# Performance work log

Hardware: AMD Instinct MI355X
Metric: run time of the kernel (lower is better)

## Reference

```python
import jax, jax.numpy as jnp
import numpy as np

H = 256
B = 4096          # number of graphs / motifs in batch
NF = 131072       # focal atoms
NR = 262144       # residues
V = 8001          # vocab.size() + 1
TOPK = 5
DIST_THRESH = 6.0


def setup_inputs() -> dict:
    key = jax.random.key(0)
    ks = jax.random.split(key, 12)
    h_ctx_focal = jax.random.normal(ks[0], (NF, H), dtype=jnp.float32)
    pos_ctx_focal = jax.random.normal(ks[1], (NF, 3), dtype=jnp.float32)
    current_wid = jax.random.randint(ks[2], (B,), 0, V)
    current_atoms_batch = jnp.sort(jax.random.randint(ks[3], (NF,), 0, B))
    h_residue = jax.random.normal(ks[4], (NR, H), dtype=jnp.float32)
    residue_pos = jax.random.normal(ks[5], (NR, 3, 3), dtype=jnp.float32)
    amino_acid_batch = jnp.sort(jax.random.randint(ks[6], (NR,), 0, B))
    emb_weight = jax.random.normal(ks[7], (V, H), dtype=jnp.float32) * 0.02
    mlp_w1 = jax.random.normal(ks[8], (3 * H, H), dtype=jnp.float32) * (1.0 / np.sqrt(3 * H))
    mlp_b1 = jnp.zeros((H,), dtype=jnp.float32)
    mlp_w2 = jax.random.normal(ks[9], (H, H), dtype=jnp.float32) * (1.0 / np.sqrt(H))
    mlp_b2 = jnp.zeros((H,), dtype=jnp.float32)
    return {
        'h_ctx_focal': h_ctx_focal, 'pos_ctx_focal': pos_ctx_focal,
        'current_wid': current_wid, 'current_atoms_batch': current_atoms_batch,
        'h_residue': h_residue, 'residue_pos': residue_pos,
        'amino_acid_batch': amino_acid_batch, 'emb_weight': emb_weight,
        'mlp_w1': mlp_w1, 'mlp_b1': mlp_b1, 'mlp_w2': mlp_w2, 'mlp_b2': mlp_b2,
    }


def reference(h_ctx_focal, pos_ctx_focal, current_wid, current_atoms_batch,
              h_residue, residue_pos, amino_acid_batch,
              emb_weight, mlp_w1, mlp_b1, mlp_w2, mlp_b2):
    nB = current_wid.shape[0]
    # scatter_add over focal atoms -> [B, H]
    node_hiddens = jax.ops.segment_sum(h_ctx_focal, current_atoms_batch, num_segments=nB)
    # embedding lookup -> [B, H]
    motif_hiddens = emb_weight[current_wid]
    # scatter_mean of positions -> [B, 3]
    pos_sum = jax.ops.segment_sum(pos_ctx_focal, current_atoms_batch, num_segments=nB)
    counts = jax.ops.segment_sum(jnp.ones((pos_ctx_focal.shape[0],), jnp.float32),
                                 current_atoms_batch, num_segments=nB)
    center_pos = pos_sum / jnp.maximum(counts, 1.0)[:, None]
    # CA position of each residue, distance mask (< 6 A from motif center)
    ca_pos = residue_pos[:, 1, :]                                  # [NR, 3]
    dist = jnp.linalg.norm(ca_pos - center_pos[amino_acid_batch], axis=1)
    mask = dist < DIST_THRESH                                      # [NR]
    # masked scatter_add of residue embeddings -> [B, H]
    residue_emb = jax.ops.segment_sum(jnp.where(mask[:, None], h_residue, 0.0),
                                      amino_acid_batch, num_segments=nB)
    # motif MLP (2 layers) + projection onto embedding table
    pred_vecs = jnp.concatenate([node_hiddens, motif_hiddens, residue_emb], axis=-1)  # [B, 3H]
    h = jax.nn.relu(pred_vecs @ mlp_w1 + mlp_b1)
    mh = h @ mlp_w2 + mlp_b2                                        # [B, H]
    pred_scores = mh @ emb_weight.T                                 # [B, V]
    # top-k + random selection among top-k
    _, select_pool = jax.lax.top_k(pred_scores, TOPK)               # [B, k]
    idx = jax.random.randint(jax.random.key(1), (nB,), 0, TOPK)
    preds = jnp.take_along_axis(select_pool, idx[:, None], axis=1)[:, 0]
    return (pred_scores, preds)
```

## Files before the change

kernel.cpp:

```cpp
#include <hip/hip_runtime.h>
#include <hip/hip_bf16.h>
#include <cstdint>

#define HD   256
#define BSZ  4096
#define NFV  131072
#define NRV  262144
#define VV   8001
#define TOPKN 5
#define RBOFF (BSZ + 1)
#define EPAD 8064

typedef __attribute__((ext_vector_type(8))) short short8v;
typedef __attribute__((ext_vector_type(4))) float float4v;

__host__ __device__ __forceinline__ unsigned rotl32(unsigned v, int d) {
  return (v << d) | (v >> (32 - d));
}

__host__ __device__ __forceinline__ void threefry2x32(
    unsigned k0, unsigned k1, unsigned x0, unsigned x1,
    unsigned& o0, unsigned& o1) {
  unsigned ks2 = k0 ^ k1 ^ 0x1BD11BDAu;
  x0 += k0; x1 += k1;
  x0 += x1; x1 = rotl32(x1, 13); x1 ^= x0;
  x0 += x1; x1 = rotl32(x1, 15); x1 ^= x0;
  x0 += x1; x1 = rotl32(x1, 26); x1 ^= x0;
  x0 += x1; x1 = rotl32(x1,  6); x1 ^= x0;
  x0 += k1; x1 += ks2 + 1u;
  x0 += x1; x1 = rotl32(x1, 17); x1 ^= x0;
  x0 += x1; x1 = rotl32(x1, 29); x1 ^= x0;
  x0 += x1; x1 = rotl32(x1, 16); x1 ^= x0;
  x0 += x1; x1 = rotl32(x1, 24); x1 ^= x0;
  x0 += ks2; x1 += k0 + 2u;
  x0 += x1; x1 = rotl32(x1, 13); x1 ^= x0;
  x0 += x1; x1 = rotl32(x1, 15); x1 ^= x0;
  x0 += x1; x1 = rotl32(x1, 26); x1 ^= x0;
  x0 += x1; x1 = rotl32(x1,  6); x1 ^= x0;
  x0 += k0; x1 += k1 + 3u;
  x0 += x1; x1 = rotl32(x1, 17); x1 ^= x0;
  x0 += x1; x1 = rotl32(x1, 29); x1 ^= x0;
  x0 += x1; x1 = rotl32(x1, 16); x1 ^= x0;
  x0 += x1; x1 = rotl32(x1, 24); x1 ^= x0;
  x0 += k1; x1 += ks2 + 4u;
  x0 += x1; x1 = rotl32(x1, 13); x1 ^= x0;
  x0 += x1; x1 = rotl32(x1, 15); x1 ^= x0;
  x0 += x1; x1 = rotl32(x1, 26); x1 ^= x0;
  x0 += x1; x1 = rotl32(x1,  6); x1 ^= x0;
  x0 += ks2; x1 += k0 + 5u;
  o0 = x0; o1 = x1;
}

__device__ __forceinline__ unsigned short f2bf(float f) {
  unsigned u = __float_as_uint(f);
  unsigned r = (u + 0x7FFFu + ((u >> 16) & 1u)) >> 16;
  return (unsigned short)r;
}
__device__ __forceinline__ float bf2f(unsigned short s) {
  return __uint_as_float(((unsigned)s) << 16);
}

__device__ __forceinline__ int lower_bound_i(const int* __restrict__ a, int n, int v) {
  int lo = 0, hi = n;
  while (lo < hi) { int m = (lo + hi) >> 1; if (a[m] < v) lo = m + 1; else hi = m; }
  return lo;
}

__global__ __launch_bounds__(256) void seg_bounds_kernel(
    const int* __restrict__ ab, const int* __restrict__ rb,
    int* __restrict__ bounds) {
  int i = blockIdx.x * 256 + threadIdx.x;
  if (i <= BSZ) bounds[i] = lower_bound_i(ab, NFV, i);
  else if (i <= 2 * BSZ + 1) bounds[i] = lower_bound_i(rb, NRV, i - RBOFF);
}

__global__ __launch_bounds__(256) void convert_emb_kernel(
    const float* __restrict__ emb, unsigned short* __restrict__ ehi,
    unsigned short* __restrict__ elo) {
  size_t i = ((size_t)blockIdx.x * 256 + threadIdx.x) * 4;
  int row = (int)(i >> 8);
  float f[4] = {0.f, 0.f, 0.f, 0.f};
  if (row < VV) {
    float4 v = *reinterpret_cast<const float4*>(&emb[i]);
    f[0] = v.x; f[1] = v.y; f[2] = v.z; f[3] = v.w;
  }
  unsigned short h[4], l[4];
#pragma unroll
  for (int j = 0; j < 4; ++j) {
    h[j] = f2bf(f[j]);
    l[j] = f2bf(f[j] - bf2f(h[j]));
  }
  *reinterpret_cast<uint2*>(&ehi[i]) = *reinterpret_cast<uint2*>(h);
  *reinterpret_cast<uint2*>(&elo[i]) = *reinterpret_cast<uint2*>(l);
}

__global__ __launch_bounds__(256) void mask_kernel(
    const float* __restrict__ pcf, const float* __restrict__ rpos,
    const int* __restrict__ bounds, unsigned char* __restrict__ mask) {
  int lane = threadIdx.x & 63;
  int b = blockIdx.x * 4 + (threadIdx.x >> 6);
  int a0 = bounds[b], a1 = bounds[b + 1];
  int r0 = bounds[RBOFF + b], r1 = bounds[RBOFF + b + 1];

  float cp = 0.f;
  if (lane < 3 && a0 < a1) {
    float nv = pcf[(size_t)a0 * 3 + lane];
    for (int aa = a0; aa < a1; ++aa) {
      float cv = nv;
      if (aa + 1 < a1) nv = pcf[(size_t)(aa + 1) * 3 + lane];
      cp += cv;
    }
  }
  if (lane < 3) cp = cp / fmaxf((float)(a1 - a0), 1.0f);
  float cx = __shfl(cp, 0), cy = __shfl(cp, 1), cz = __shfl(cp, 2);

  for (int r = r0 + lane; r < r1; r += 64) {
    float dx = rpos[(size_t)r * 9 + 3] - cx;
    float dy = rpos[(size_t)r * 9 + 4] - cy;
    float dz = rpos[(size_t)r * 9 + 5] - cz;
    mask[r] = (dx * dx + dy * dy + dz * dz < 36.0f) ? 1 : 0;
  }
}

__global__ __launch_bounds__(256) void fuse_seg_kernel(
    const float* __restrict__ hcf, const int* __restrict__ wid,
    const float* __restrict__ hres, const unsigned char* __restrict__ mask,
    const float* __restrict__ emb, const int* __restrict__ bounds,
    float* __restrict__ pred_vecs) {
  int lane = threadIdx.x & 63;
  int b = blockIdx.x * 4 + (threadIdx.x >> 6);
  int a0 = bounds[b], a1 = bounds[b + 1];
  int r0 = bounds[RBOFF + b], r1 = bounds[RBOFF + b + 1];
  size_t off = (size_t)lane * 4;

  float4v acc = 0.f;
  int a = a0;
  for (; a + 8 <= a1; a += 8) {
    float4v v[8];
#pragma unroll
    for (int j = 0; j < 8; ++j)
      v[j] = *reinterpret_cast<const float4v*>(&hcf[(size_t)(a + j) * HD + off]);
    acc += ((v[0] + v[1]) + (v[2] + v[3])) + ((v[4] + v[5]) + (v[6] + v[7]));
  }
  for (; a < a1; ++a)
    acc += *reinterpret_cast<const float4v*>(&hcf[(size_t)a * HD + off]);

  size_t o = (size_t)b * (3 * HD);
  *reinterpret_cast<float4v*>(&pred_vecs[o + off]) = acc;
  float4v mv = *reinterpret_cast<const float4v*>(&emb[(size_t)wid[b] * HD + off]);
  *reinterpret_cast<float4v*>(&pred_vecs[o + HD + off]) = mv;

  float4v racc = 0.f;
  int r = r0;
  for (; r < r1 && (r & 7); ++r) {
    float4v v = *reinterpret_cast<const float4v*>(&hres[(size_t)r * HD + off]);
    if (mask[r]) racc += v;
  }
  for (; r + 8 <= r1; r += 8) {
    uint2 mw = *reinterpret_cast<const uint2*>(&mask[r]);
    float4v v[8];
#pragma unroll
    for (int j = 0; j < 8; ++j)
      v[j] = *reinterpret_cast<const float4v*>(&hres[(size_t)(r + j) * HD + off]);
    float4v s0 = 0.f, s1 = 0.f, s2 = 0.f, s3 = 0.f;
    if (mw.x & 0x000000FFu) s0 += v[0];
    if (mw.x & 0x0000FF00u) s1 += v[1];
    if (mw.x & 0x00FF0000u) s2 += v[2];
    if (mw.x & 0xFF000000u) s3 += v[3];
    if (mw.y & 0x000000FFu) s0 += v[4];
    if (mw.y & 0x0000FF00u) s1 += v[5];
    if (mw.y & 0x00FF0000u) s2 += v[6];
    if (mw.y & 0xFF000000u) s3 += v[7];
    racc += (s0 + s1) + (s2 + s3);
  }
  for (; r < r1; ++r) {
    float4v v = *reinterpret_cast<const float4v*>(&hres[(size_t)r * HD + off]);
    if (mask[r]) racc += v;
  }
  *reinterpret_cast<float4v*>(&pred_vecs[o + 2 * HD + off]) = racc;
}

template <bool RELU, bool SPLIT>
__global__ __launch_bounds__(256) void gemm_kernel(
    const float* __restrict__ A, const float* __restrict__ B,
    const float* __restrict__ bias, float* __restrict__ C,
    unsigned short* __restrict__ Chi, unsigned short* __restrict__ Clo,
    int M, int N, int K) {
  __shared__ float As[16][64];
  __shared__ float Bs[16][64];
  int t = threadIdx.x;
  int bm = blockIdx.y * 64, bn = blockIdx.x * 64;
  int tx = t & 15, ty = t >> 4;
  float acc[4][4] = {};

  for (int k0 = 0; k0 < K; k0 += 16) {
    {
      int ar = t >> 2, ak = (t & 3) << 2;
      float4 av = *reinterpret_cast<const float4*>(&A[(size_t)(bm + ar) * K + k0 + ak]);
      As[ak + 0][ar] = av.x; As[ak + 1][ar] = av.y;
      As[ak + 2][ar] = av.z; As[ak + 3][ar] = av.w;
    }
    {
      int bk = t >> 4, bnn = (t & 15) << 2;
      float4 bv = *reinterpret_cast<const float4*>(&B[(size_t)(k0 + bk) * N + bn + bnn]);
      *reinterpret_cast<float4*>(&Bs[bk][bnn]) = bv;
    }
    __syncthreads();
#pragma unroll
    for (int kk = 0; kk < 16; ++kk) {
      float4 a = *reinterpret_cast<const float4*>(&As[kk][ty << 2]);
      float4 b = *reinterpret_cast<const float4*>(&Bs[kk][tx << 2]);
      float av4[4] = {a.x, a.y, a.z, a.w};
      float bv4[4] = {b.x, b.y, b.z, b.w};
#pragma unroll
      for (int i = 0; i < 4; ++i)
#pragma unroll
        for (int j = 0; j < 4; ++j)
          acc[i][j] = fmaf(av4[i], bv4[j], acc[i][j]);
    }
    __syncthreads();
  }

#pragma unroll
  for (int i = 0; i < 4; ++i) {
    int row = bm + (ty << 2) + i;
    if (SPLIT) {
      unsigned short h[4], l[4];
#pragma unroll
      for (int j = 0; j < 4; ++j) {
        float v = acc[i][j] + bias[bn + (tx << 2) + j];
        h[j] = f2bf(v);
        l[j] = f2bf(v - bf2f(h[j]));
      }
      size_t base = (size_t)row * N + bn + (tx << 2);
      *reinterpret_cast<uint2*>(&Chi[base]) = *reinterpret_cast<uint2*>(h);
      *reinterpret_cast<uint2*>(&Clo[base]) = *reinterpret_cast<uint2*>(l);
    } else {
#pragma unroll
      for (int j = 0; j < 4; ++j) {
        int col = bn + (tx << 2) + j;
        float v = acc[i][j] + bias[col];
        if (RELU) v = fmaxf(v, 0.f);
        C[(size_t)row * N + col] = v;
      }
    }
  }
}

#define SW(row, col) ((col) ^ (((row) & 7) << 3))

__global__ __launch_bounds__(256, 2) void score_gemm_kernel(
    const unsigned short* __restrict__ Ahg, const unsigned short* __restrict__ Alg,
    const unsigned short* __restrict__ Bhg, const unsigned short* __restrict__ Blg,
    float* __restrict__ C) {
  __shared__ __attribute__((aligned(16))) unsigned short Ah[128 * 64];
  __shared__ __attribute__((aligned(16))) unsigned short Al[128 * 64];
  __shared__ __attribute__((aligned(16))) unsigned short Bh[128 * 64];
  __shared__ __attribute__((aligned(16))) unsigned short Bl[128 * 64];

  int t = threadIdx.x;
  int bm = blockIdx.x * 128;
  int bn = blockIdx.y * 128;
  int lane = t & 63, wv = t >> 6;
  int wm = wv >> 1, wn = wv & 1;
  int lr = lane & 15, lg = lane >> 4;

  float4v acc[4][4] = {};

  int srow = t >> 1, scol = (t & 1) * 32;

  for (int kb = 0; kb < 256; kb += 64) {
#pragma unroll
    for (int j = 0; j < 4; ++j) {
      int c = scol + j * 8;
      int li = srow * 64 + SW(srow, c);
      size_t ga = (size_t)(bm + srow) * 256 + kb + c;
      size_t gb = (size_t)(bn + srow) * 256 + kb + c;
      *reinterpret_cast<short8v*>(&Ah[li]) = *reinterpret_cast<const short8v*>(&Ahg[ga]);
      *reinterpret_cast<short8v*>(&Al[li]) = *reinterpret_cast<const short8v*>(&Alg[ga]);
      *reinterpret_cast<short8v*>(&Bh[li]) = *reinterpret_cast<const short8v*>(&Bhg[gb]);
      *reinterpret_cast<short8v*>(&Bl[li]) = *reinterpret_cast<const short8v*>(&Blg[gb]);
    }
    __syncthreads();

#pragma unroll
    for (int ks = 0; ks < 2; ++ks) {
      int ko = ks * 32 + lg * 8;
      short8v aH[4], aL[4], bH[4], bL[4];
#pragma unroll
      for (int f = 0; f < 4; ++f) {
        int ra = wm * 64 + f * 16 + lr;
        int rb2 = wn * 64 + f * 16 + lr;
        aH[f] = *reinterpret_cast<const short8v*>(&Ah[ra * 64 + SW(ra, ko)]);
        aL[f] = *reinterpret_cast<const short8v*>(&Al[ra * 64 + SW(ra, ko)]);
        bH[f] = *reinterpret_cast<const short8v*>(&Bh[rb2 * 64 + SW(rb2, ko)]);
        bL[f] = *reinterpret_cast<const short8v*>(&Bl[rb2 * 64 + SW(rb2, ko)]);
      }
#pragma unroll
      for (int mf = 0; mf < 4; ++mf)
#pragma unroll
        for (int nf = 0; nf < 4; ++nf) {
          acc[mf][nf] = __builtin_amdgcn_mfma_f32_16x16x32_bf16(
              aH[mf], bH[nf], acc[mf][nf], 0, 0, 0);
          acc[mf][nf] = __builtin_amdgcn_mfma_f32_16x16x32_bf16(
              aH[mf], bL[nf], acc[mf][nf], 0, 0, 0);
          acc[mf][nf] = __builtin_amdgcn_mfma_f32_16x16x32_bf16(
              aL[mf], bH[nf], acc[mf][nf], 0, 0, 0);
        }
    }
    __syncthreads();
  }

#pragma unroll
  for (int mf = 0; mf < 4; ++mf)
#pragma unroll
    for (int nf = 0; nf < 4; ++nf) {
      int col = bn + wn * 64 + nf * 16 + lr;
      if (col < VV) {
#pragma unroll
        for (int rr = 0; rr < 4; ++rr) {
          int row = bm + wm * 64 + mf * 16 + lg * 4 + rr;
          C[(size_t)row * VV + col] = acc[mf][nf][rr];
        }
      }
    }
}

#define BETTER(av, ai, bv, bi) ((av) > (bv) || ((av) == (bv) && (ai) < (bi)))

__global__ __launch_bounds__(256) void topk_kernel(
    const float* __restrict__ scores, float* __restrict__ preds,
    unsigned k1a, unsigned k1b, unsigned k2a, unsigned k2b) {
  int lane = threadIdx.x & 63;
  int row = (blockIdx.x << 2) + (threadIdx.x >> 6);
  const float* s = scores + (size_t)row * VV;

  const float NEG = -__builtin_huge_valf();
  float v0 = NEG, v1 = NEG, v2 = NEG, v3 = NEG, v4 = NEG;
  int i0 = 0x7FFFFFFF, i1 = 0x7FFFFFFF, i2 = 0x7FFFFFFF, i3 = 0x7FFFFFFF, i4 = 0x7FFFFFFF;

  for (int v = lane; v < VV; v += 64) {
    float val = s[v];
    if (BETTER(val, v, v4, i4)) {
      if (BETTER(val, v, v3, i3)) {
        v4 = v3; i4 = i3;
        if (BETTER(val, v, v2, i2)) {
          v3 = v2; i3 = i2;
          if (BETTER(val, v, v1, i1)) {
            v2 = v1; i2 = i1;
            if (BETTER(val, v, v0, i0)) {
              v1 = v0; i1 = i0; v0 = val; i0 = v;
            } else { v1 = val; i1 = v; }
          } else { v2 = val; i2 = v; }
        } else { v3 = val; i3 = v; }
      } else { v4 = val; i4 = v; }
    }
  }

  int sel0, sel1, sel2, sel3, sel4;
#pragma unroll
  for (int p = 0; p < TOPKN; ++p) {
    float bv = v0; int bi = i0;
#pragma unroll
    for (int off = 32; off > 0; off >>= 1) {
      float ov = __shfl_xor(bv, off);
      int   oi = __shfl_xor(bi, off);
      if (BETTER(ov, oi, bv, bi)) { bv = ov; bi = oi; }
    }
    if (p == 0) sel0 = bi; else if (p == 1) sel1 = bi; else if (p == 2) sel2 = bi;
    else if (p == 3) sel3 = bi; else sel4 = bi;
    if (bi == i0) {
      v0 = v1; i0 = i1; v1 = v2; i1 = i2; v2 = v3; i2 = i3; v3 = v4; i3 = i4;
      v4 = NEG; i4 = 0x7FFFFFFF;
    }
  }

  if (lane == 0) {
    unsigned i = (unsigned)row;
    unsigned h0, h1, l0, l1;
    threefry2x32(k1a, k1b, 0u, i, h0, h1);
    threefry2x32(k2a, k2b, 0u, i, l0, l1);
    unsigned hb = h0 ^ h1;
    unsigned lb = l0 ^ l1;
    unsigned idx = ((hb % 5u) + (lb % 5u)) % 5u;
    int pick = (idx == 0) ? sel0 : (idx == 1) ? sel1 : (idx == 2) ? sel2
             : (idx == 3) ? sel3 : sel4;
    preds[row] = (float)pick;
  }
}

extern "C" void kernel_launch(void* const* d_in, const int* in_sizes, int n_in,
                              void* d_out, int out_size, void* d_ws, size_t ws_size,
                              hipStream_t stream) {
  const float* hcf  = (const float*)d_in[0];
  const float* pcf  = (const float*)d_in[1];
  const int*   wid  = (const int*)d_in[2];
  const int*   ab   = (const int*)d_in[3];
  const float* hres = (const float*)d_in[4];
  const float* rpos = (const float*)d_in[5];
  const int*   rb   = (const int*)d_in[6];
  const float* emb  = (const float*)d_in[7];
  const float* w1   = (const float*)d_in[8];
  const float* bb1  = (const float*)d_in[9];
  const float* w2   = (const float*)d_in[10];
  const float* bb2  = (const float*)d_in[11];

  float* out    = (float*)d_out;
  float* scores = out;
  float* preds  = out + (size_t)BSZ * VV;

  float* pred_vecs = out;
  float* hbuf      = out + (size_t)BSZ * 768;

  char* ws = (char*)d_ws;
  int*            bounds = (int*)(ws);
  unsigned char*  mask   = (unsigned char*)(ws + 0x10000);
  unsigned short* mh_hi  = (unsigned short*)(ws + 0x100000);
  unsigned short* mh_lo  = (unsigned short*)(ws + 0x300000);
  unsigned short* emb_hi = (unsigned short*)(ws + 0x500000);
  unsigned short* emb_lo = (unsigned short*)(ws + 0x900000);

  seg_bounds_kernel<<<(2 * (BSZ + 1) + 255) / 256, 256, 0, stream>>>(ab, rb, bounds);

  convert_emb_kernel<<<(EPAD * 256 / 4) / 256, 256, 0, stream>>>(emb, emb_hi, emb_lo);

  mask_kernel<<<BSZ / 4, 256, 0, stream>>>(pcf, rpos, bounds, mask);

  fuse_seg_kernel<<<BSZ / 4, 256, 0, stream>>>(
      hcf, wid, hres, mask, emb, bounds, pred_vecs);

  gemm_kernel<true, false><<<dim3(256 / 64, BSZ / 64), 256, 0, stream>>>(
      pred_vecs, w1, bb1, hbuf, nullptr, nullptr, BSZ, 256, 768);
  gemm_kernel<false, true><<<dim3(256 / 64, BSZ / 64), 256, 0, stream>>>(
      hbuf, w2, bb2, nullptr, mh_hi, mh_lo, BSZ, 256, 256);

  score_gemm_kernel<<<dim3(BSZ / 128, (VV + 127) / 128), 256, 0, stream>>>(
      mh_hi, mh_lo, emb_hi, emb_lo, scores);

  unsigned k1a, k1b, k2a, k2b;
  threefry2x32(0u, 1u, 0u, 0u, k1a, k1b);
  threefry2x32(0u, 1u, 0u, 1u, k2a, k2b);
  topk_kernel<<<BSZ / 4, 256, 0, stream>>>(scores, preds, k1a, k1b, k2a, k2b);
}
```

Measured before the change: 344.6 us.

## Move MLP GEMMs to split-bf16 MFMA and use direct global-to-LDS loads

Replaces the two fp32 SIMT MLP GEMMs with MFMA kernels that take operands split into bf16 hi/lo parts. The segment-sum kernel now writes pred_vecs already split, and the weights are transposed and split inside a new combined prep kernel that also absorbs the bounds and embedding conversion launches. The score GEMM switches to global_load_lds for direct-to-LDS staging and drops the XOR swizzle, which may bring back LDS bank conflicts. The three-product split-bf16 scheme slightly changes the arithmetic compared with fp32 FMA.

```diff
diff --git a/kernel.cpp b/kernel.cpp
--- a/kernel.cpp
+++ b/kernel.cpp
@@ -66,32 +66,54 @@
   return lo;
 }
 
-__global__ __launch_bounds__(256) void seg_bounds_kernel(
-    const int* __restrict__ ab, const int* __restrict__ rb,
-    int* __restrict__ bounds) {
-  int i = blockIdx.x * 256 + threadIdx.x;
-  if (i <= BSZ) bounds[i] = lower_bound_i(ab, NFV, i);
-  else if (i <= 2 * BSZ + 1) bounds[i] = lower_bound_i(rb, NRV, i - RBOFF);
-}
-
-__global__ __launch_bounds__(256) void convert_emb_kernel(
+__device__ __forceinline__ void gl16(const unsigned short* g, unsigned short* l) {
+  __builtin_amdgcn_global_load_lds(
+      (const __attribute__((address_space(1))) unsigned int*)g,
+      (__attribute__((address_space(3))) unsigned int*)l, 16, 0, 0);
+}
+
+__global__ __launch_bounds__(256) void prep_kernel(
+    const int* __restrict__ ab, const int* __restrict__ rb, int* __restrict__ bounds,
     const float* __restrict__ emb, unsigned short* __restrict__ ehi,
-    unsigned short* __restrict__ elo) {
-  size_t i = ((size_t)blockIdx.x * 256 + threadIdx.x) * 4;
-  int row = (int)(i >> 8);
-  float f[4] = {0.f, 0.f, 0.f, 0.f};
-  if (row < VV) {
-    float4 v = *reinterpret_cast<const float4*>(&emb[i]);
-    f[0] = v.x; f[1] = v.y; f[2] = v.z; f[3] = v.w;
-  }
-  unsigned short h[4], l[4];
-#pragma unroll
-  for (int j = 0; j < 4; ++j) {
-    h[j] = f2bf(f[j]);
-    l[j] = f2bf(f[j] - bf2f(h[j]));
-  }
-  *reinterpret_cast<uint2*>(&ehi[i]) = *reinterpret_cast<uint2*>(h);
-  *reinterpret_cast<uint2*>(&elo[i]) = *reinterpret_cast<uint2*>(l);
+    unsigned short* __restrict__ elo,
+    const float* __restrict__ w1, unsigned short* __restrict__ w1th,
+    unsigned short* __restrict__ w1tl,
+    const float* __restrict__ w2, unsigned short* __restrict__ w2th,
+    unsigned short* __restrict__ w2tl) {
+  int blk = blockIdx.x, t = threadIdx.x;
+  if (blk < 33) {
+    int i = blk * 256 + t;
+    if (i <= BSZ) bounds[i] = lower_bound_i(ab, NFV, i);
+    else if (i <= 2 * BSZ + 1) bounds[i] = lower_bound_i(rb, NRV, i - RBOFF);
+  } else if (blk < 33 + 2016) {
+    size_t i = ((size_t)(blk - 33) * 256 + t) * 4;
+    int row = (int)(i >> 8);
+    float f[4] = {0.f, 0.f, 0.f, 0.f};
+    if (row < VV) {
+      float4 v = *reinterpret_cast<const float4*>(&emb[i]);
+      f[0] = v.x; f[1] = v.y; f[2] = v.z; f[3] = v.w;
+    }
+    unsigned short h[4], l[4];
+#pragma unroll
+    for (int j = 0; j < 4; ++j) {
+      h[j] = f2bf(f[j]);
+      l[j] = f2bf(f[j] - bf2f(h[j]));
+    }
+    *reinterpret_cast<uint2*>(&ehi[i]) = *reinterpret_cast<uint2*>(h);
+    *reinterpret_cast<uint2*>(&elo[i]) = *reinterpret_cast<uint2*>(l);
+  } else if (blk < 33 + 2016 + 768) {
+    int i = (blk - 2049) * 256 + t;
+    int n = i / 768, k = i - n * 768;
+    float v = w1[k * 256 + n];
+    unsigned short h = f2bf(v);
+    w1th[i] = h; w1tl[i] = f2bf(v - bf2f(h));
+  } else {
+    int i = (blk - 2817) * 256 + t;
+    int n = i >> 8, k = i & 255;
+    float v = w2[k * 256 + n];
+    unsigned short h = f2bf(v);
+    w2th[i] = h; w2tl[i] = f2bf(v - bf2f(h));
+  }
 }
 
 __global__ __launch_bounds__(256) void mask_kernel(
@@ -125,8 +147,9 @@
 __global__ __launch_bounds__(256) void fuse_seg_kernel(
     const float* __restrict__ hcf, const int* __restrict__ wid,
     const float* __restrict__ hres, const unsigned char* __restrict__ mask,
-    const float* __restrict__ emb, const int* __restrict__ bounds,
-    float* __restrict__ pred_vecs) {
+    const unsigned short* __restrict__ ehi, const unsigned short* __restrict__ elo,
+    const int* __restrict__ bounds,
+    unsigned short* __restrict__ pvh, unsigned short* __restrict__ pvl) {
   int lane = threadIdx.x & 63;
   int b = blockIdx.x * 4 + (threadIdx.x >> 6);
   int a0 = bounds[b], a1 = bounds[b + 1];
@@ -144,11 +167,6 @@
   }
   for (; a < a1; ++a)
     acc += *reinterpret_cast<const float4v*>(&hcf[(size_t)a * HD + off]);
-
-  size_t o = (size_t)b * (3 * HD);
-  *reinterpret_cast<float4v*>(&pred_vecs[o + off]) = acc;
-  float4v mv = *reinterpret_cast<const float4v*>(&emb[(size_t)wid[b] * HD + off]);
-  *reinterpret_cast<float4v*>(&pred_vecs[o + HD + off]) = mv;
 
   float4v racc = 0.f;
   int r = r0;
@@ -177,77 +195,108 @@
     float4v v = *reinterpret_cast<const float4v*>(&hres[(size_t)r * HD + off]);
     if (mask[r]) racc += v;
   }
-  *reinterpret_cast<float4v*>(&pred_vecs[o + 2 * HD + off]) = racc;
-}
-
-template <bool RELU, bool SPLIT>
-__global__ __launch_bounds__(256) void gemm_kernel(
-    const float* __restrict__ A, const float* __restrict__ B,
-    const float* __restrict__ bias, float* __restrict__ C,
-    unsigned short* __restrict__ Chi, unsigned short* __restrict__ Clo,
-    int M, int N, int K) {
-  __shared__ float As[16][64];
-  __shared__ float Bs[16][64];
+
+  size_t o = (size_t)b * 768;
+  {
+    unsigned short h[4], l[4];
+#pragma unroll
+    for (int j = 0; j < 4; ++j) {
+      h[j] = f2bf(acc[j]); l[j] = f2bf(acc[j] - bf2f(h[j]));
+    }
+    *reinterpret_cast<uint2*>(&pvh[o + off]) = *reinterpret_cast<uint2*>(h);
+    *reinterpret_cast<uint2*>(&pvl[o + off]) = *reinterpret_cast<uint2*>(l);
+  }
+  *reinterpret_cast<uint2*>(&pvh[o + 256 + off]) =
+      *reinterpret_cast<const uint2*>(&ehi[(size_t)wid[b] * 256 + off]);
+  *reinterpret_cast<uint2*>(&pvl[o + 256 + off]) =
+      *reinterpret_cast<const uint2*>(&elo[(size_t)wid[b] * 256 + off]);
+  {
+    unsigned short h[4], l[4];
+#pragma unroll
+    for (int j = 0; j < 4; ++j) {
+      h[j] = f2bf(racc[j]); l[j] = f2bf(racc[j] - bf2f(h[j]));
+    }
+    *reinterpret_cast<uint2*>(&pvh[o + 512 + off]) = *reinterpret_cast<uint2*>(h);
+    *reinterpret_cast<uint2*>(&pvl[o + 512 + off]) = *reinterpret_cast<uint2*>(l);
+  }
+}
+
+template <bool RELU, int K, int N>
+__global__ __launch_bounds__(256) void mlp_gemm_kernel(
+    const unsigned short* __restrict__ Ahg, const unsigned short* __restrict__ Alg,
+    const unsigned short* __restrict__ Bhg, const unsigned short* __restrict__ Blg,
+    const float* __restrict__ bias,
+    unsigned short* __restrict__ Chi, unsigned short* __restrict__ Clo) {
+  __shared__ __attribute__((aligned(16))) unsigned short Ahs[64][72];
+  __shared__ __attribute__((aligned(16))) unsigned short Als[64][72];
+  __shared__ __attribute__((aligned(16))) unsigned short Bhs[64][72];
+  __shared__ __attribute__((aligned(16))) unsigned short Bls[64][72];
+
   int t = threadIdx.x;
   int bm = blockIdx.y * 64, bn = blockIdx.x * 64;
-  int tx = t & 15, ty = t >> 4;
-  float acc[4][4] = {};
-
-  for (int k0 = 0; k0 < K; k0 += 16) {
-    {
-      int ar = t >> 2, ak = (t & 3) << 2;
-      float4 av = *reinterpret_cast<const float4*>(&A[(size_t)(bm + ar) * K + k0 + ak]);
-      As[ak + 0][ar] = av.x; As[ak + 1][ar] = av.y;
-      As[ak + 2][ar] = av.z; As[ak + 3][ar] = av.w;
-    }
-    {
-      int bk = t >> 4, bnn = (t & 15) << 2;
-      float4 bv = *reinterpret_cast<const float4*>(&B[(size_t)(k0 + bk) * N + bn + bnn]);
-      *reinterpret_cast<float4*>(&Bs[bk][bnn]) = bv;
-    }
+  int lane = t & 63, wv = t >> 6;
+  int wm = wv >> 1, wn = wv & 1;
+  int lr = lane & 15, lg = lane >> 4;
+  float4v acc[2][2] = {};
+
+  int srow = t >> 2, sc = (t & 3) * 16;
+
+  for (int kb = 0; kb < K; kb += 64) {
+    size_t ga = (size_t)(bm + srow) * K + kb + sc;
+    size_t gb = (size_t)(bn + srow) * K + kb + sc;
+    *reinterpret_cast<short8v*>(&Ahs[srow][sc]) = *reinterpret_cast<const short8v*>(&Ahg[ga]);
+    *reinterpret_cast<short8v*>(&Ahs[srow][sc + 8]) = *reinterpret_cast<const short8v*>(&Ahg[ga + 8]);
+    *reinterpret_cast<short8v*>(&Als[srow][sc]) = *reinterpret_cast<const short8v*>(&Alg[ga]);
+    *reinterpret_cast<short8v*>(&Als[srow][sc + 8]) = *reinterpret_cast<const short8v*>(&Alg[ga + 8]);
+    *reinterpret_cast<short8v*>(&Bhs[srow][sc]) = *reinterpret_cast<const short8v*>(&Bhg[gb]);
+    *reinterpret_cast<short8v*>(&Bhs[srow][sc + 8]) = *reinterpret_cast<const short8v*>(&Bhg[gb + 8]);
+    *reinterpret_cast<short8v*>(&Bls[srow][sc]) = *reinterpret_cast<const short8v*>(&Blg[gb]);
+    *reinterpret_cast<short8v*>(&Bls[srow][sc + 8]) = *reinterpret_cast<const short8v*>(&Blg[gb + 8]);
     __syncthreads();
-#pragma unroll
-    for (int kk = 0; kk < 16; ++kk) {
-      float4 a = *reinterpret_cast<const float4*>(&As[kk][ty << 2]);
-      float4 b = *reinterpret_cast<const float4*>(&Bs[kk][tx << 2]);
-      float av4[4] = {a.x, a.y, a.z, a.w};
-      float bv4[4] = {b.x, b.y, b.z, b.w};
-#pragma unroll
-      for (int i = 0; i < 4; ++i)
-#pragma unroll
-        for (int j = 0; j < 4; ++j)
-          acc[i][j] = fmaf(av4[i], bv4[j], acc[i][j]);
+
+#pragma unroll
+    for (int ks = 0; ks < 2; ++ks) {
+      int ko = ks * 32 + lg * 8;
+      short8v aH[2], aL[2], bH[2], bL[2];
+#pragma unroll
+      for (int f = 0; f < 2; ++f) {
+        aH[f] = *reinterpret_cast<const short8v*>(&Ahs[wm * 32 + f * 16 + lr][ko]);
+        aL[f] = *reinterpret_cast<const short8v*>(&Als[wm * 32 + f * 16 + lr][ko]);
+        bH[f] = *reinterpret_cast<const short8v*>(&Bhs[wn * 32 + f * 16 + lr][ko]);
+        bL[f] = *reinterpret_cast<const short8v*>(&Bls[wn * 32 + f * 16 + lr][ko]);
+      }
+#pragma unroll
+      for (int mf = 0; mf < 2; ++mf)
+#pragma unroll
+        for (int nf = 0; nf < 2; ++nf) {
+          acc[mf][nf] = __builtin_amdgcn_mfma_f32_16x16x32_bf16(
+              aH[mf], bH[nf], acc[mf][nf], 0, 0, 0);
+          acc[mf][nf] = __builtin_amdgcn_mfma_f32_16x16x32_bf16(
+              aH[mf], bL[nf], acc[mf][nf], 0, 0, 0);
+          acc[mf][nf] = __builtin_amdgcn_mfma_f32_16x16x32_bf16(
+              aL[mf], bH[nf], acc[mf][nf], 0, 0, 0);
+        }
     }
     __syncthreads();
   }
 
 #pragma unroll
-  for (int i = 0; i < 4; ++i) {
-    int row = bm + (ty << 2) + i;
-    if (SPLIT) {
-      unsigned short h[4], l[4];
-#pragma unroll
-      for (int j = 0; j < 4; ++j) {
-        float v = acc[i][j] + bias[bn + (tx << 2) + j];
-        h[j] = f2bf(v);
-        l[j] = f2bf(v - bf2f(h[j]));
+  for (int mf = 0; mf < 2; ++mf)
+#pragma unroll
+    for (int nf = 0; nf < 2; ++nf) {
+      int col = bn + wn * 32 + nf * 16 + lr;
+      float bv = bias[col];
+#pragma unroll
+      for (int rr = 0; rr < 4; ++rr) {
+        int row = bm + wm * 32 + mf * 16 + lg * 4 + rr;
+        float v = acc[mf][nf][rr] + bv;
+        if (RELU) v = fmaxf(v, 0.f);
+        unsigned short h = f2bf(v);
+        Chi[(size_t)row * N + col] = h;
+        Clo[(size_t)row * N + col] = f2bf(v - bf2f(h));
       }
-      size_t base = (size_t)row * N + bn + (tx << 2);
-      *reinterpret_cast<uint2*>(&Chi[base]) = *reinterpret_cast<uint2*>(h);
-      *reinterpret_cast<uint2*>(&Clo[base]) = *reinterpret_cast<uint2*>(l);
-    } else {
-#pragma unroll
-      for (int j = 0; j < 4; ++j) {
-        int col = bn + (tx << 2) + j;
-        float v = acc[i][j] + bias[col];
-        if (RELU) v = fmaxf(v, 0.f);
-        C[(size_t)row * N + col] = v;
-      }
-    }
-  }
-}
-
-#define SW(row, col) ((col) ^ (((row) & 7) << 3))
+    }
+}
 
 __global__ __launch_bounds__(256, 2) void score_gemm_kernel(
     const unsigned short* __restrict__ Ahg, const unsigned short* __restrict__ Alg,
@@ -267,19 +316,21 @@
 
   float4v acc[4][4] = {};
 
-  int srow = t >> 1, scol = (t & 1) * 32;
+  int rsub = lane >> 3;
+  int csub = (lane & 7) * 8;
 
   for (int kb = 0; kb < 256; kb += 64) {
 #pragma unroll
     for (int j = 0; j < 4; ++j) {
-      int c = scol + j * 8;
-      int li = srow * 64 + SW(srow, c);
-      size_t ga = (size_t)(bm + srow) * 256 + kb + c;
-      size_t gb = (size_t)(bn + srow) * 256 + kb + c;
-      *reinterpret_cast<short8v*>(&Ah[li]) = *reinterpret_cast<const short8v*>(&Ahg[ga]);
-      *reinterpret_cast<short8v*>(&Al[li]) = *reinterpret_cast<const short8v*>(&Alg[ga]);
-      *reinterpret_cast<short8v*>(&Bh[li]) = *reinterpret_cast<const short8v*>(&Bhg[gb]);
-      *reinterpret_cast<short8v*>(&Bl[li]) = *reinterpret_cast<const short8v*>(&Blg[gb]);
+      int ch = wv * 4 + j;
+      int grow = ch * 8 + rsub;
+      size_t goA = (size_t)(bm + grow) * 256 + kb + csub;
+      size_t goB = (size_t)(bn + grow) * 256 + kb + csub;
+      unsigned lo = ch * 512 + lane * 8;
+      gl16(&Ahg[goA], &Ah[lo]);
+      gl16(&Alg[goA], &Al[lo]);
+      gl16(&Bhg[goB], &Bh[lo]);
+      gl16(&Blg[goB], &Bl[lo]);
     }
     __syncthreads();
 
@@ -291,10 +342,10 @@
       for (int f = 0; f < 4; ++f) {
         int ra = wm * 64 + f * 16 + lr;
         int rb2 = wn * 64 + f * 16 + lr;
-        aH[f] = *reinterpret_cast<const short8v*>(&Ah[ra * 64 + SW(ra, ko)]);
-        aL[f] = *reinterpret_cast<const short8v*>(&Al[ra * 64 + SW(ra, ko)]);
-        bH[f] = *reinterpret_cast<const short8v*>(&Bh[rb2 * 64 + SW(rb2, ko)]);
-        bL[f] = *reinterpret_cast<const short8v*>(&Bl[rb2 * 64 + SW(rb2, ko)]);
+        aH[f] = *reinterpret_cast<const short8v*>(&Ah[ra * 64 + ko]);
+        aL[f] = *reinterpret_cast<const short8v*>(&Al[ra * 64 + ko]);
+        bH[f] = *reinterpret_cast<const short8v*>(&Bh[rb2 * 64 + ko]);
+        bL[f] = *reinterpret_cast<const short8v*>(&Bl[rb2 * 64 + ko]);
       }
 #pragma unroll
       for (int mf = 0; mf < 4; ++mf)
@@ -409,8 +460,15 @@
   float* scores = out;
   float* preds  = out + (size_t)BSZ * VV;
 
-  float* pred_vecs = out;
-  float* hbuf      = out + (size_t)BSZ * 768;
+  char* ob = (char*)d_out;
+  unsigned short* pvh  = (unsigned short*)(ob);
+  unsigned short* pvl  = (unsigned short*)(ob + 0x600000);
+  unsigned short* hh   = (unsigned short*)(ob + 0xC00000);
+  unsigned short* hl   = (unsigned short*)(ob + 0xE00000);
+  unsigned short* w1th = (unsigned short*)(ob + 0x1000000);
+  unsigned short* w1tl = (unsigned short*)(ob + 0x1060000);
+  unsigned short* w2th = (unsigned short*)(ob + 0x10C0000);
+  unsigned short* w2tl = (unsigned short*)(ob + 0x10E0000);
 
   char* ws = (char*)d_ws;
   int*            bounds = (int*)(ws);
@@ -420,19 +478,18 @@
   unsigned short* emb_hi = (unsigned short*)(ws + 0x500000);
   unsigned short* emb_lo = (unsigned short*)(ws + 0x900000);
 
-  seg_bounds_kernel<<<(2 * (BSZ + 1) + 255) / 256, 256, 0, stream>>>(ab, rb, bounds);
-
-  convert_emb_kernel<<<(EPAD * 256 / 4) / 256, 256, 0, stream>>>(emb, emb_hi, emb_lo);
+  prep_kernel<<<33 + 2016 + 768 + 256, 256, 0, stream>>>(
+      ab, rb, bounds, emb, emb_hi, emb_lo, w1, w1th, w1tl, w2, w2th, w2tl);
 
   mask_kernel<<<BSZ / 4, 256, 0, stream>>>(pcf, rpos, bounds, mask);
 
   fuse_seg_kernel<<<BSZ / 4, 256, 0, stream>>>(
-      hcf, wid, hres, mask, emb, bounds, pred_vecs);
-
-  gemm_kernel<true, false><<<dim3(256 / 64, BSZ / 64), 256, 0, stream>>>(
-      pred_vecs, w1, bb1, hbuf, nullptr, nullptr, BSZ, 256, 768);
-  gemm_kernel<false, true><<<dim3(256 / 64, BSZ / 64), 256, 0, stream>>>(
-      hbuf, w2, bb2, nullptr, mh_hi, mh_lo, BSZ, 256, 256);
+      hcf, wid, hres, mask, emb_hi, emb_lo, bounds, pvh, pvl);
+
+  mlp_gemm_kernel<true, 768, 256><<<dim3(4, 64), 256, 0, stream>>>(
+      pvh, pvl, w1th, w1tl, bb1, hh, hl);
+  mlp_gemm_kernel<false, 256, 256><<<dim3(4, 64), 256, 0, stream>>>(
+      hh, hl, w2th, w2tl, bb2, mh_hi, mh_lo);
 
   score_gemm_kernel<<<dim3(BSZ / 128, (VV + 127) / 128), 256, 0, stream>>>(
       mh_hi, mh_lo, emb_hi, emb_lo, scores);
```

After: 295.9 us. -14.1%, faster.
